# Optimization experiments

Hardware: AMD Instinct MI355X
Metric: run time of the kernel (lower is better)

Reference implementation:

```python
import jax, jax.numpy as jnp
import numpy as np

BRIGHT_THRESH = 0.65
SAT_THRESH = 0.15
SMOOTH_K = 15
LAMBDA_L1 = 1.0
LAMBDA_WIN_L1 = 3.0
LAMBDA_WIN_COLOR = 1.0
WINDOW_WEIGHT = 5.0
BASE_WEIGHT = 1.0
TRANSFORM_WEIGHT = 2.0
EPS = 1e-8


def _avg_pool_same(x, k=SMOOTH_K):
    # AvgPool2d(k, stride=1, padding=k//2), count_include_pad=True (torch default)
    p = k // 2
    s = jax.lax.reduce_window(x, 0.0, jax.lax.add, (1, 1, k, k), (1, 1, 1, 1),
                              [(0, 0), (0, 0), (p, p), (p, p)])
    return s / (k * k)


def _window_detector(source):
    # Rescale from [-1,1] to [0,1] if any negative values present
    src = jnp.where(source.min() < 0, (source + 1) * 0.5, source)
    brightness = 0.299 * src[:, 0:1] + 0.587 * src[:, 1:2] + 0.114 * src[:, 2:3]
    bright_mask = jax.nn.sigmoid(20.0 * (brightness - BRIGHT_THRESH))
    saturation = src.max(axis=1, keepdims=True) - src.min(axis=1, keepdims=True)
    low_sat_mask = jax.nn.sigmoid(20.0 * (SAT_THRESH - saturation))
    return _avg_pool_same(bright_mask * low_sat_mask)


def _normalize_ch(x):
    # F.normalize over channel dim with eps clamp
    n = jnp.sqrt(jnp.sum(x * x, axis=1, keepdims=True))
    return x / jnp.maximum(n, EPS)


def setup_inputs() -> dict:
    key = jax.random.key(0)
    k1, k2, k3 = jax.random.split(key, 3)
    shape = (16, 3, 512, 512)
    return {
        "pred": jax.random.normal(k1, shape, dtype=jnp.float32),
        "target": jax.random.normal(k2, shape, dtype=jnp.float32),
        "source": jax.random.normal(k3, shape, dtype=jnp.float32),
    }


def reference(pred, target, source):
    window_mask = _window_detector(source)  # [B,1,H,W]

    # plain L1
    l1_loss = jnp.abs(pred - target).mean()

    # window-weighted L1
    weight_map = BASE_WEIGHT + (WINDOW_WEIGHT - BASE_WEIGHT) * window_mask
    win_l1_loss = (jnp.abs(pred - target) * weight_map).mean()

    # window color-transform loss
    st = target - source  # source -> target direction
    sp = pred - source    # source -> pred direction
    alignment = jnp.sum(_normalize_ch(st) * _normalize_ch(sp), axis=1, keepdims=True)
    st_mag = jnp.sqrt(jnp.sum(st * st, axis=1, keepdims=True))
    sp_mag = jnp.sqrt(jnp.sum(sp * sp, axis=1, keepdims=True))
    mag_loss = jnp.abs(sp_mag / (st_mag + EPS) - 1.0)
    color_loss = TRANSFORM_WEIGHT * (window_mask * (1.0 - alignment + 0.5 * mag_loss)).mean()

    total = LAMBDA_L1 * l1_loss + LAMBDA_WIN_L1 * win_l1_loss + LAMBDA_WIN_COLOR * color_loss
    return total
```

## Files before the change

kernel.cpp:

```cpp
#include <hip/hip_runtime.h>
#include <math.h>

#define W 512
#define H 512
#define BATCH 16
#define HW (W * H)
#define NPIX (BATCH * HW)
#define NELEM (3 * NPIX)

#define TWT 64
#define THT 16
#define NTILES 4096
#define WPB 4
#define NBLOCKS (NTILES / WPB)

#define MR 30
#define MC 80
#define NHQ (MR * 16)
#define NHALO 344
#define WLDS (MR * MC)

__device__ __forceinline__ float fast_rcp(float x)  { return __builtin_amdgcn_rcpf(x); }
__device__ __forceinline__ float fast_sqrt(float x) { return __builtin_amdgcn_sqrtf(x); }

__device__ __forceinline__ float maskval(float r, float g, float b) {
    const float R = (r + 1.f) * 0.5f;
    const float G = (g + 1.f) * 0.5f;
    const float B = (b + 1.f) * 0.5f;
    const float bright = 0.299f * R + 0.587f * G + 0.114f * B;
    const float sat = fmaxf(R, fmaxf(G, B)) - fminf(R, fminf(G, B));
    const float bm = fast_rcp(1.f + __expf(-20.f * (bright - 0.65f)));
    const float sm = fast_rcp(1.f + __expf(-20.f * (0.15f - sat)));
    return bm * sm;
}

__device__ __forceinline__ float4 maskval4(float4 R4, float4 G4, float4 B4) {
    float4 m;
    m.x = maskval(R4.x, G4.x, B4.x);
    m.y = maskval(R4.y, G4.y, B4.y);
    m.z = maskval(R4.z, G4.z, B4.z);
    m.w = maskval(R4.w, G4.w, B4.w);
    return m;
}

__device__ __forceinline__ void loss4(const float4& pR, const float4& pG, const float4& pB,
                                      const float4& tR, const float4& tG, const float4& tB,
                                      const float4& sR, const float4& sG, const float4& sB,
                                      const float4& Sw, float& sA, float& sAW, float& sC) {
    const float inv225 = 1.f / 225.f;
    const float wm[4] = {Sw.x * inv225, Sw.y * inv225, Sw.z * inv225, Sw.w * inv225};
    const float pr[4] = {pR.x, pR.y, pR.z, pR.w}, pg[4] = {pG.x, pG.y, pG.z, pG.w},
                pb[4] = {pB.x, pB.y, pB.z, pB.w};
    const float tr[4] = {tR.x, tR.y, tR.z, tR.w}, tg[4] = {tG.x, tG.y, tG.z, tG.w},
                tb[4] = {tB.x, tB.y, tB.z, tB.w};
    const float sr[4] = {sR.x, sR.y, sR.z, sR.w}, sg[4] = {sG.x, sG.y, sG.z, sG.w},
                sb[4] = {sB.x, sB.y, sB.z, sB.w};
#pragma unroll
    for (int j = 0; j < 4; ++j) {
        const float a = fabsf(pr[j] - tr[j]) + fabsf(pg[j] - tg[j]) + fabsf(pb[j] - tb[j]);
        const float stx = tr[j] - sr[j], sty = tg[j] - sg[j], stz = tb[j] - sb[j];
        const float spx = pr[j] - sr[j], spy = pg[j] - sg[j], spz = pb[j] - sb[j];
        const float dot = stx * spx + sty * spy + stz * spz;
        const float stm = fast_sqrt(stx * stx + sty * sty + stz * stz);
        const float spm = fast_sqrt(spx * spx + spy * spy + spz * spz);
        const float align = dot * fast_rcp(fmaxf(stm, 1e-8f) * fmaxf(spm, 1e-8f));
        const float mag = fabsf(spm * fast_rcp(stm + 1e-8f) - 1.f);
        const float c = 1.f - align + 0.5f * mag;
        sA  += a;
        sAW += a * wm[j];
        sC  += c * wm[j];
    }
}

struct Row9 {
    float4 pR, pG, pB, tR, tG, tB, sR, sG, sB;
};

__device__ __forceinline__ void load_row(Row9& r, const float* __restrict__ pred,
                                         const float* __restrict__ targ,
                                         const float* __restrict__ srcp, size_t o) {
    r.pR = *(const float4*)(pred + o);
    r.pG = *(const float4*)(pred + o + HW);
    r.pB = *(const float4*)(pred + o + 2 * HW);
    r.tR = *(const float4*)(targ + o);
    r.tG = *(const float4*)(targ + o + HW);
    r.tB = *(const float4*)(targ + o + 2 * HW);
    r.sR = *(const float4*)(srcp + o);
    r.sG = *(const float4*)(srcp + o + HW);
    r.sB = *(const float4*)(srcp + o + 2 * HW);
}

__device__ __forceinline__ void loss_row(const Row9& r, const float4& S,
                                         float& sA, float& sAW, float& sC) {
    loss4(r.pR, r.pG, r.pB, r.tR, r.tG, r.tB, r.sR, r.sG, r.sB, S, sA, sAW, sC);
}

__attribute__((amdgpu_waves_per_eu(4, 4)))
__global__ __launch_bounds__(256) void k_fused(const float* __restrict__ pred,
                                               const float* __restrict__ targ,
                                               const float* __restrict__ srcp,
                                               float* __restrict__ partials) {
    __shared__ __align__(16) float lds[WPB * WLDS];

    const int tid  = threadIdx.x;
    const int raw  = blockIdx.x;
    const int bid  = ((raw & 7) << 7) | (raw >> 3);
    const int wv   = tid >> 6;
    const int lane = tid & 63;
    const int tile = bid * WPB + wv;
    const int img  = tile >> 8;
    const int tl   = tile & 255;
    const int y0   = (tl >> 3) * THT;
    const int x0   = (tl & 7) * TWT;
    const size_t ibase = (size_t)img * 3 * HW;
    float* buf = lds + wv * WLDS;

    const int r4 = lane >> 4;
    const int q  = lane & 15;
    const size_t cb = ibase + (size_t)(y0 + 4 * r4) * W + (x0 + 4 * q);

    {
        const float4 c0r = *(const float4*)(srcp + cb);
        const float4 c0g = *(const float4*)(srcp + cb + HW);
        const float4 c0b = *(const float4*)(srcp + cb + 2 * HW);
        const float4 c1r = *(const float4*)(srcp + cb + W);
        const float4 c1g = *(const float4*)(srcp + cb + W + HW);
        const float4 c1b = *(const float4*)(srcp + cb + W + 2 * HW);
        const float4 c2r = *(const float4*)(srcp + cb + 2 * W);
        const float4 c2g = *(const float4*)(srcp + cb + 2 * W + HW);
        const float4 c2b = *(const float4*)(srcp + cb + 2 * W + 2 * HW);
        const float4 c3r = *(const float4*)(srcp + cb + 3 * W);
        const float4 c3g = *(const float4*)(srcp + cb + 3 * W + HW);
        const float4 c3b = *(const float4*)(srcp + cb + 3 * W + 2 * HW);
        float* crow = buf + (7 + 4 * r4) * MC + 8 + 4 * q;
        *(float4*)(crow)          = maskval4(c0r, c0g, c0b);
        *(float4*)(crow + MC)     = maskval4(c1r, c1g, c1b);
        *(float4*)(crow + 2 * MC) = maskval4(c2r, c2g, c2b);
        *(float4*)(crow + 3 * MC) = maskval4(c3r, c3g, c3b);
    }

#pragma unroll
    for (int it = 0; it < 6; ++it) {
        const int p = it * 64 + lane;
        if (p < NHALO) {
            int smr, hq;
            if (p < 280) {
                const int hr = p / 20;
                smr = (hr < 7) ? hr : hr + 16;
                hq  = p - hr * 20;
            } else {
                const int j = p - 280;
                smr = (j >> 2) + 7;
                const int k = j & 3;
                hq  = (k < 2) ? k : k + 16;
            }
            const int gy = y0 - 7 + smr;
            const int gx = x0 - 8 + 4 * hq;
            const bool valid = ((unsigned)gy < (unsigned)H) && ((unsigned)gx < (unsigned)W);
            const size_t o = valid ? (ibase + (size_t)gy * W + gx) : ibase;
            const float4 A = *(const float4*)(srcp + o);
            const float4 B = *(const float4*)(srcp + o + HW);
            const float4 C = *(const float4*)(srcp + o + 2 * HW);
            float4 mv = maskval4(A, B, C);
            if (!valid) mv = make_float4(0.f, 0.f, 0.f, 0.f);
            *(float4*)(buf + smr * MC + 4 * hq) = mv;
        }
    }

#pragma unroll
    for (int i = 0; i < 8; ++i) {
        const int p = i * 64 + lane;
        if (p < NHQ) {
            const int r  = p >> 4;
            const int qq = p & 15;
            float* mr = buf + r * MC + 4 * qq;
            const float4 v0 = *(const float4*)(mr);
            const float4 v1 = *(const float4*)(mr + 4);
            const float4 v2 = *(const float4*)(mr + 8);
            const float4 v3 = *(const float4*)(mr + 12);
            const float4 v4 = *(const float4*)(mr + 16);
            const float mid = v1.x + v1.y + v1.z + v1.w
                            + v2.x + v2.y + v2.z + v2.w
                            + v3.x + v3.y + v3.z + v3.w;
            float4 h;
            h.x = v0.y + v0.z + v0.w + mid;
            h.y = h.x - v0.y + v4.x;
            h.z = h.y - v0.z + v4.y;
            h.w = h.z - v0.w + v4.z;
            *(float4*)(mr) = h;
        }
    }

    const float* hcol = buf + 4 * q;
    const int rb = 4 * r4;

    Row9 rA, rB;
    load_row(rA, pred, targ, srcp, cb);

    const float4 h0 = *(const float4*)(hcol + (rb + 0) * MC);
    const float4 h1 = *(const float4*)(hcol + (rb + 1) * MC);
    const float4 h2 = *(const float4*)(hcol + (rb + 2) * MC);
    float4 S0 = make_float4(h0.x + h1.x + h2.x, h0.y + h1.y + h2.y,
                            h0.z + h1.z + h2.z, h0.w + h1.w + h2.w);
#pragma unroll
    for (int k = 3; k < 15; ++k) {
        const float4 hv = *(const float4*)(hcol + (rb + k) * MC);
        S0.x += hv.x; S0.y += hv.y; S0.z += hv.z; S0.w += hv.w;
    }

    float sA = 0.f, sAW = 0.f, sC = 0.f;

    load_row(rB, pred, targ, srcp, cb + W);
    loss_row(rA, S0, sA, sAW, sC);

    load_row(rA, pred, targ, srcp, cb + 2 * W);
    const float4 a15 = *(const float4*)(hcol + (rb + 15) * MC);
    const float4 S1 = make_float4(S0.x - h0.x + a15.x, S0.y - h0.y + a15.y,
                                  S0.z - h0.z + a15.z, S0.w - h0.w + a15.w);
    loss_row(rB, S1, sA, sAW, sC);

    load_row(rB, pred, targ, srcp, cb + 3 * W);
    const float4 a16 = *(const float4*)(hcol + (rb + 16) * MC);
    const float4 S2 = make_float4(S1.x - h1.x + a16.x, S1.y - h1.y + a16.y,
                                  S1.z - h1.z + a16.z, S1.w - h1.w + a16.w);
    loss_row(rA, S2, sA, sAW, sC);

    const float4 a17 = *(const float4*)(hcol + (rb + 17) * MC);
    const float4 S3 = make_float4(S2.x - h2.x + a17.x, S2.y - h2.y + a17.y,
                                  S2.z - h2.z + a17.z, S2.w - h2.w + a17.w);
    loss_row(rB, S3, sA, sAW, sC);

#pragma unroll
    for (int off = 32; off > 0; off >>= 1) {
        sA  += __shfl_down(sA, off);
        sAW += __shfl_down(sAW, off);
        sC  += __shfl_down(sC, off);
    }
    if (lane == 0) {
        partials[(size_t)tile * 3 + 0] = sA;
        partials[(size_t)tile * 3 + 1] = sAW;
        partials[(size_t)tile * 3 + 2] = sC;
    }
}

__global__ __launch_bounds__(256) void k_final(const float* __restrict__ partials,
                                               float* __restrict__ out) {
    double a = 0.0, aw = 0.0, c = 0.0;
    for (int i = threadIdx.x; i < NTILES; i += 256) {
        a  += (double)partials[(size_t)i * 3 + 0];
        aw += (double)partials[(size_t)i * 3 + 1];
        c  += (double)partials[(size_t)i * 3 + 2];
    }
#pragma unroll
    for (int off = 32; off > 0; off >>= 1) {
        a  += __shfl_down(a, off);
        aw += __shfl_down(aw, off);
        c  += __shfl_down(c, off);
    }
    __shared__ double rd[3][4];
    const int lane = threadIdx.x & 63;
    const int wave = threadIdx.x >> 6;
    if (lane == 0) { rd[0][wave] = a; rd[1][wave] = aw; rd[2][wave] = c; }
    __syncthreads();
    if (threadIdx.x == 0) {
        const double A  = rd[0][0] + rd[0][1] + rd[0][2] + rd[0][3];
        const double AW = rd[1][0] + rd[1][1] + rd[1][2] + rd[1][3];
        const double C  = rd[2][0] + rd[2][1] + rd[2][2] + rd[2][3];
        const double N = (double)NELEM;
        const double M = (double)NPIX;
        out[0] = (float)((4.0 * A + 12.0 * AW) / N + 2.0 * C / M);
    }
}

extern "C" void kernel_launch(void* const* d_in, const int* in_sizes, int n_in,
                              void* d_out, int out_size, void* d_ws, size_t ws_size,
                              hipStream_t stream) {
    const float* pred = (const float*)d_in[0];
    const float* targ = (const float*)d_in[1];
    const float* src  = (const float*)d_in[2];

    float* partials = (float*)d_ws;

    k_fused<<<NBLOCKS, 256, 0, stream>>>(pred, targ, src, partials);
    k_final<<<1, 256, 0, stream>>>(partials, (float*)d_out);
}
```

Before: 175.9 us.

## Stream taller tiles through an LDS ring buffer for the vertical box sum

Tile height doubles from 16 to 32 rows. The window mask is now built in 4-row steps: each step computes the mask and horizontal sums for the next rows and writes them into a 20-row LDS ring, and loss rows are computed once their 15-row vertical window is ready. This cuts the share of halo rows re-reading source, and shrinks per-wave LDS. In exchange each row does 15 LDS reads instead of a sliding update, occupancy is limited to 2 waves per EU, and there are fewer tiles in flight.

After: 295.4 us. +68.0%, slower.

```diff
diff --git a/kernel.cpp b/kernel.cpp
--- a/kernel.cpp
+++ b/kernel.cpp
@@ -9,16 +9,16 @@
 #define NELEM (3 * NPIX)
 
 #define TWT 64
-#define THT 16
-#define NTILES 4096
+#define THT 32
+#define NTILES 2048
 #define WPB 4
 #define NBLOCKS (NTILES / WPB)
 
-#define MR 30
-#define MC 80
-#define NHQ (MR * 16)
-#define NHALO 344
-#define WLDS (MR * MC)
+#define MB 80
+#define RR 20
+#define RC 64
+#define WLDS (4 * MB + RR * RC)
+#define NSTEP 12
 
 __device__ __forceinline__ float fast_rcp(float x)  { return __builtin_amdgcn_rcpf(x); }
 __device__ __forceinline__ float fast_sqrt(float x) { return __builtin_amdgcn_sqrtf(x); }
@@ -90,145 +90,110 @@
     r.sB = *(const float4*)(srcp + o + 2 * HW);
 }
 
-__device__ __forceinline__ void loss_row(const Row9& r, const float4& S,
-                                         float& sA, float& sAW, float& sC) {
-    loss4(r.pR, r.pG, r.pB, r.tR, r.tG, r.tB, r.sR, r.sG, r.sB, S, sA, sAW, sC);
-}
-
-__attribute__((amdgpu_waves_per_eu(4, 4)))
-__global__ __launch_bounds__(256) void k_fused(const float* __restrict__ pred,
-                                               const float* __restrict__ targ,
-                                               const float* __restrict__ srcp,
-                                               float* __restrict__ partials) {
+__device__ __forceinline__ void mask_step(const float* __restrict__ srcp, size_t ibase,
+                                          float* mbuf, float* ring,
+                                          int y0, int x0, int r4, int q, int lane,
+                                          int s, int smod) {
+    const int my = y0 - 7 + 4 * s + r4;
+    const bool vrow = (unsigned)my < (unsigned)H;
+    const int myc = vrow ? my : 0;
+
+    const size_t oc = ibase + (size_t)myc * W + (x0 + 4 * q);
+    const float4 cr = *(const float4*)(srcp + oc);
+    const float4 cg = *(const float4*)(srcp + oc + HW);
+    const float4 cb = *(const float4*)(srcp + oc + 2 * HW);
+    *(float4*)(mbuf + r4 * MB + 8 + 4 * q) = maskval4(cr, cg, cb);
+
+    if (lane < 16) {
+        const int hr4 = lane >> 2;
+        const int hk  = lane & 3;
+        const int myh = y0 - 7 + 4 * s + hr4;
+        const int gxh = (hk < 2) ? (x0 - 8 + 4 * hk) : (x0 + 56 + 4 * hk);
+        const bool vh = ((unsigned)myh < (unsigned)H) && ((unsigned)gxh < (unsigned)W);
+        const size_t oh = vh ? (ibase + (size_t)myh * W + gxh) : ibase;
+        const float4 ar = *(const float4*)(srcp + oh);
+        const float4 ag = *(const float4*)(srcp + oh + HW);
+        const float4 ab = *(const float4*)(srcp + oh + 2 * HW);
+        float4 mh = maskval4(ar, ag, ab);
+        if (!vh) mh = make_float4(0.f, 0.f, 0.f, 0.f);
+        const int hc = hr4 * MB + ((hk < 2) ? 4 * hk : 64 + 4 * hk);
+        *(float4*)(mbuf + hc) = mh;
+    }
+
+    const float* mr = mbuf + r4 * MB + 4 * q;
+    const float4 v0 = *(const float4*)(mr);
+    const float4 v1 = *(const float4*)(mr + 4);
+    const float4 v2 = *(const float4*)(mr + 8);
+    const float4 v3 = *(const float4*)(mr + 12);
+    const float4 v4 = *(const float4*)(mr + 16);
+    const float mid = v1.x + v1.y + v1.z + v1.w
+                    + v2.x + v2.y + v2.z + v2.w
+                    + v3.x + v3.y + v3.z + v3.w;
+    float4 h;
+    h.x = v0.y + v0.z + v0.w + mid;
+    h.y = h.x - v0.y + v4.x;
+    h.z = h.y - v0.z + v4.y;
+    h.w = h.z - v0.w + v4.z;
+    if (!vrow) h = make_float4(0.f, 0.f, 0.f, 0.f);
+    *(float4*)(ring + (smod + r4) * RC + 4 * q) = h;
+}
+
+__attribute__((amdgpu_waves_per_eu(2, 2)))
+__global__ __launch_bounds__(256, 2) void k_fused(const float* __restrict__ pred,
+                                                  const float* __restrict__ targ,
+                                                  const float* __restrict__ srcp,
+                                                  float* __restrict__ partials) {
     __shared__ __align__(16) float lds[WPB * WLDS];
 
     const int tid  = threadIdx.x;
     const int raw  = blockIdx.x;
-    const int bid  = ((raw & 7) << 7) | (raw >> 3);
+    const int bid  = ((raw & 7) << 6) | (raw >> 3);
     const int wv   = tid >> 6;
     const int lane = tid & 63;
     const int tile = bid * WPB + wv;
-    const int img  = tile >> 8;
-    const int tl   = tile & 255;
+    const int img  = tile >> 7;
+    const int tl   = tile & 127;
     const int y0   = (tl >> 3) * THT;
     const int x0   = (tl & 7) * TWT;
     const size_t ibase = (size_t)img * 3 * HW;
-    float* buf = lds + wv * WLDS;
+
+    float* mbuf = lds + wv * WLDS;
+    float* ring = mbuf + 4 * MB;
 
     const int r4 = lane >> 4;
     const int q  = lane & 15;
-    const size_t cb = ibase + (size_t)(y0 + 4 * r4) * W + (x0 + 4 * q);
-
-    {
-        const float4 c0r = *(const float4*)(srcp + cb);
-        const float4 c0g = *(const float4*)(srcp + cb + HW);
-        const float4 c0b = *(const float4*)(srcp + cb + 2 * HW);
-        const float4 c1r = *(const float4*)(srcp + cb + W);
-        const float4 c1g = *(const float4*)(srcp + cb + W + HW);
-        const float4 c1b = *(const float4*)(srcp + cb + W + 2 * HW);
-        const float4 c2r = *(const float4*)(srcp + cb + 2 * W);
-        const float4 c2g = *(const float4*)(srcp + cb + 2 * W + HW);
-        const float4 c2b = *(const float4*)(srcp + cb + 2 * W + 2 * HW);
-        const float4 c3r = *(const float4*)(srcp + cb + 3 * W);
-        const float4 c3g = *(const float4*)(srcp + cb + 3 * W + HW);
-        const float4 c3b = *(const float4*)(srcp + cb + 3 * W + 2 * HW);
-        float* crow = buf + (7 + 4 * r4) * MC + 8 + 4 * q;
-        *(float4*)(crow)          = maskval4(c0r, c0g, c0b);
-        *(float4*)(crow + MC)     = maskval4(c1r, c1g, c1b);
-        *(float4*)(crow + 2 * MC) = maskval4(c2r, c2g, c2b);
-        *(float4*)(crow + 3 * MC) = maskval4(c3r, c3g, c3b);
-    }
-
-#pragma unroll
-    for (int it = 0; it < 6; ++it) {
-        const int p = it * 64 + lane;
-        if (p < NHALO) {
-            int smr, hq;
-            if (p < 280) {
-                const int hr = p / 20;
-                smr = (hr < 7) ? hr : hr + 16;
-                hq  = p - hr * 20;
-            } else {
-                const int j = p - 280;
-                smr = (j >> 2) + 7;
-                const int k = j & 3;
-                hq  = (k < 2) ? k : k + 16;
-            }
-            const int gy = y0 - 7 + smr;
-            const int gx = x0 - 8 + 4 * hq;
-            const bool valid = ((unsigned)gy < (unsigned)H) && ((unsigned)gx < (unsigned)W);
-            const size_t o = valid ? (ibase + (size_t)gy * W + gx) : ibase;
-            const float4 A = *(const float4*)(srcp + o);
-            const float4 B = *(const float4*)(srcp + o + HW);
-            const float4 C = *(const float4*)(srcp + o + 2 * HW);
-            float4 mv = maskval4(A, B, C);
-            if (!valid) mv = make_float4(0.f, 0.f, 0.f, 0.f);
-            *(float4*)(buf + smr * MC + 4 * hq) = mv;
+
+    float sA = 0.f, sAW = 0.f, sC = 0.f;
+
+    mask_step(srcp, ibase, mbuf, ring, y0, x0, r4, q, lane, 0, 0);
+    mask_step(srcp, ibase, mbuf, ring, y0, x0, r4, q, lane, 1, 4);
+    mask_step(srcp, ibase, mbuf, ring, y0, x0, r4, q, lane, 2, 8);
+    mask_step(srcp, ibase, mbuf, ring, y0, x0, r4, q, lane, 3, 12);
+
+    int smod = 16;
+    int cmod = 0;
+#pragma unroll
+    for (int s = 4; s < NSTEP; ++s) {
+        mask_step(srcp, ibase, mbuf, ring, y0, x0, r4, q, lane, s, smod);
+        smod += 4; if (smod >= 20) smod -= 20;
+
+        const int c = s - 4;
+        const size_t ob = ibase + (size_t)(y0 + 4 * c + r4) * W + (x0 + 4 * q);
+        Row9 r;
+        load_row(r, pred, targ, srcp, ob);
+
+        float4 S = make_float4(0.f, 0.f, 0.f, 0.f);
+#pragma unroll
+        for (int k = 0; k < 15; ++k) {
+            int sl = cmod + r4 + k;
+            if (sl >= 20) sl -= 20;
+            const float4 hv = *(const float4*)(ring + sl * RC + 4 * q);
+            S.x += hv.x; S.y += hv.y; S.z += hv.z; S.w += hv.w;
         }
-    }
-
-#pragma unroll
-    for (int i = 0; i < 8; ++i) {
-        const int p = i * 64 + lane;
-        if (p < NHQ) {
-            const int r  = p >> 4;
-            const int qq = p & 15;
-            float* mr = buf + r * MC + 4 * qq;
-            const float4 v0 = *(const float4*)(mr);
-            const float4 v1 = *(const float4*)(mr + 4);
-            const float4 v2 = *(const float4*)(mr + 8);
-            const float4 v3 = *(const float4*)(mr + 12);
-            const float4 v4 = *(const float4*)(mr + 16);
-            const float mid = v1.x + v1.y + v1.z + v1.w
-                            + v2.x + v2.y + v2.z + v2.w
-                            + v3.x + v3.y + v3.z + v3.w;
-            float4 h;
-            h.x = v0.y + v0.z + v0.w + mid;
-            h.y = h.x - v0.y + v4.x;
-            h.z = h.y - v0.z + v4.y;
-            h.w = h.z - v0.w + v4.z;
-            *(float4*)(mr) = h;
-        }
-    }
-
-    const float* hcol = buf + 4 * q;
-    const int rb = 4 * r4;
-
-    Row9 rA, rB;
-    load_row(rA, pred, targ, srcp, cb);
-
-    const float4 h0 = *(const float4*)(hcol + (rb + 0) * MC);
-    const float4 h1 = *(const float4*)(hcol + (rb + 1) * MC);
-    const float4 h2 = *(const float4*)(hcol + (rb + 2) * MC);
-    float4 S0 = make_float4(h0.x + h1.x + h2.x, h0.y + h1.y + h2.y,
-                            h0.z + h1.z + h2.z, h0.w + h1.w + h2.w);
-#pragma unroll
-    for (int k = 3; k < 15; ++k) {
-        const float4 hv = *(const float4*)(hcol + (rb + k) * MC);
-        S0.x += hv.x; S0.y += hv.y; S0.z += hv.z; S0.w += hv.w;
-    }
-
-    float sA = 0.f, sAW = 0.f, sC = 0.f;
-
-    load_row(rB, pred, targ, srcp, cb + W);
-    loss_row(rA, S0, sA, sAW, sC);
-
-    load_row(rA, pred, targ, srcp, cb + 2 * W);
-    const float4 a15 = *(const float4*)(hcol + (rb + 15) * MC);
-    const float4 S1 = make_float4(S0.x - h0.x + a15.x, S0.y - h0.y + a15.y,
-                                  S0.z - h0.z + a15.z, S0.w - h0.w + a15.w);
-    loss_row(rB, S1, sA, sAW, sC);
-
-    load_row(rB, pred, targ, srcp, cb + 3 * W);
-    const float4 a16 = *(const float4*)(hcol + (rb + 16) * MC);
-    const float4 S2 = make_float4(S1.x - h1.x + a16.x, S1.y - h1.y + a16.y,
-                                  S1.z - h1.z + a16.z, S1.w - h1.w + a16.w);
-    loss_row(rA, S2, sA, sAW, sC);
-
-    const float4 a17 = *(const float4*)(hcol + (rb + 17) * MC);
-    const float4 S3 = make_float4(S2.x - h2.x + a17.x, S2.y - h2.y + a17.y,
-                                  S2.z - h2.z + a17.z, S2.w - h2.w + a17.w);
-    loss_row(rB, S3, sA, sAW, sC);
+        cmod += 4; if (cmod >= 20) cmod -= 20;
+
+        loss4(r.pR, r.pG, r.pB, r.tR, r.tG, r.tB, r.sR, r.sG, r.sB, S, sA, sAW, sC);
+    }
 
 #pragma unroll
     for (int off = 32; off > 0; off >>= 1) {
```
